# Kernel optimization log

Measured on AMD Instinct MI355X. Metric: run time of the kernel, lower is better.

## Reference

```python
import jax, jax.numpy as jnp
import numpy as np

N, NF1, NF2, NH, OUT, K = 16384, 2000, 10000, 512, 16, 19
BN_EPS = 1e-5

def _bn(x, g, b, m, v):
    # eval-mode BatchNorm1d with running stats
    return (x - m) * jax.lax.rsqrt(v + BN_EPS) * g + b


def setup_inputs() -> dict:
    key = jax.random.key(0)
    ks = jax.random.split(key, 24)
    f32 = jnp.float32
    def w(k, shape):
        return jax.random.normal(k, shape, f32) * 0.02
    inp = {
        "rna": jax.random.normal(ks[0], (N, NF1), f32),
        "atac": jax.random.normal(ks[1], (N, NF2), f32),
        "index_rna": jnp.arange(N, dtype=jnp.int32),
        "index_atac": jnp.arange(N, dtype=jnp.int32),
        "eps": jax.random.normal(ks[2], (N, OUT), f32),
        # RNA encoder
        "W_r1": w(ks[3], (NH, NF1)), "b_r1": jnp.zeros((NH,), f32),
        "g_r": jnp.ones((NH,), f32), "be_r": jnp.zeros((NH,), f32),
        "m_r": jnp.zeros((NH,), f32), "v_r": jnp.ones((NH,), f32),
        "W_rmu": w(ks[4], (OUT, NH)), "b_rmu": jnp.zeros((OUT,), f32),
        "W_rvar": w(ks[5], (OUT, NH)), "b_rvar": jnp.zeros((OUT,), f32),
        # ATAC encoder
        "W_a1": w(ks[6], (NH, NF2)), "b_a1": jnp.zeros((NH,), f32),
        "g_a": jnp.ones((NH,), f32), "be_a": jnp.zeros((NH,), f32),
        "m_a": jnp.zeros((NH,), f32), "v_a": jnp.ones((NH,), f32),
        "W_amu": w(ks[7], (OUT, NH)), "b_amu": jnp.zeros((OUT,), f32),
        "W_avar": w(ks[8], (OUT, NH)), "b_avar": jnp.zeros((OUT,), f32),
        # decoder
        "W_d1": w(ks[9], (NH, OUT)), "b_d1": jnp.zeros((NH,), f32),
        "g_d": jnp.ones((NH,), f32), "be_d": jnp.zeros((NH,), f32),
        "m_d": jnp.zeros((NH,), f32), "v_d": jnp.ones((NH,), f32),
        "W_d4": w(ks[10], (NF1 + NF2, NH)), "b_d4": jnp.zeros((NF1 + NF2,), f32),
        "cluster": jax.random.normal(ks[11], (K, OUT), f32),
    }
    return inp


def reference(rna, atac, index_rna, index_atac, eps,
              W_r1, b_r1, g_r, be_r, m_r, v_r, W_rmu, b_rmu, W_rvar, b_rvar,
              W_a1, b_a1, g_a, be_a, m_a, v_a, W_amu, b_amu, W_avar, b_avar,
              W_d1, b_d1, g_d, be_d, m_d, v_d, W_d4, b_d4, cluster):
    n = rna.shape[0]
    # encoders (dropout is identity in eval mode)
    h_rna = jax.nn.relu(_bn(rna @ W_r1.T + b_r1, g_r, be_r, m_r, v_r))
    zm_rna = h_rna @ W_rmu.T + b_rmu
    zv_rna = jnp.exp(h_rna @ W_rvar.T + b_rvar)
    h_atac = jax.nn.relu(_bn(atac @ W_a1.T + b_a1, g_a, be_a, m_a, v_a))
    zm_atac = h_atac @ W_amu.T + b_amu
    zv_atac = jnp.exp(h_atac @ W_avar.T + b_avar)
    # vectorized scatter replacing the per-sample Python loop
    mu = jnp.ones((n, 2, OUT), rna.dtype)
    var = jnp.ones((n, 2, OUT), rna.dtype)
    mask = jnp.zeros((n, 2, OUT), rna.dtype)
    mu = mu.at[index_rna, 0].set(zm_rna).at[index_atac, 1].set(zm_atac)
    var = var.at[index_rna, 0].set(zv_rna).at[index_atac, 1].set(zv_atac)
    mask = mask.at[index_rna, 0].set(1.0).at[index_atac, 1].set(1.0)
    # product of experts over the modality axis (axis=1)
    T = mask / var
    T_sum = T.sum(axis=1) + 1.0            # [n, OUT]
    z_mu = (mu * T).sum(axis=1) / T_sum
    z_var = 1.0 / T_sum
    # Normal(z_mu, scale=z_var).rsample() with externally supplied eps
    z = z_mu + z_var * eps
    # student-t style soft assignment to clusters
    d2 = jnp.sum((z[:, None, :] - cluster[None, :, :]) ** 2, axis=2)  # [n, K]
    q = 1.0 / (1.0 + d2)
    q = q / q.sum(axis=1, keepdims=True)
    # decoder
    h = jax.nn.relu(_bn(z @ W_d1.T + b_d1, g_d, be_d, m_d, v_d))
    recon_x = h @ W_d4.T + b_d4
    return (recon_x, z_mu, z_var, z, q)
```

## Files before the change

### kernel.cpp

```cpp
#include <hip/hip_runtime.h>
#include <hip/hip_bf16.h>

#define NS    16384
#define NF1c  2000
#define NF2c  10000
#define NH    512
#define KC    19
#define NREC  12000
#define NRECP 12032

typedef short bf16x8 __attribute__((ext_vector_type(8)));
typedef float f32x4  __attribute__((ext_vector_type(4)));

__device__ __forceinline__ unsigned short f2bf(float x) {
    return __builtin_bit_cast(unsigned short, __hip_bfloat16(x));
}
__device__ __forceinline__ float bf2f(unsigned short h) {
    return __builtin_bit_cast(float, (unsigned int)h << 16);
}

__device__ __forceinline__ void sync_nodrain() {
    asm volatile("s_waitcnt lgkmcnt(0)" ::: "memory");
    __builtin_amdgcn_s_barrier();
    asm volatile("" ::: "memory");
}

template<int BK> __device__ __forceinline__ int swz(int r) {
    return (BK == 32) ? ((r >> 1) & 3) : (r & 7);
}

__device__ __forceinline__ void gload16(const unsigned short* g, unsigned short* l) {
    __builtin_amdgcn_global_load_lds(
        (const __attribute__((address_space(1))) void*)g,
        (__attribute__((address_space(3))) void*)l, 16, 0, 0);
}

__global__ void k_cvt(const float* __restrict__ s, unsigned short* __restrict__ d, int n4) {
    int i = blockIdx.x * blockDim.x + threadIdx.x;
    int st = gridDim.x * blockDim.x;
    for (; i < n4; i += st) {
        float4 f = ((const float4*)s)[i];
        ushort4 o;
        o.x = f2bf(f.x); o.y = f2bf(f.y); o.z = f2bf(f.z); o.w = f2bf(f.w);
        ((ushort4*)d)[i] = o;
    }
}

__global__ void k_cvt_pad(const float* __restrict__ s, unsigned short* __restrict__ d,
                          int K, int Rv, long nchunks) {
    long i = (long)blockIdx.x * blockDim.x + threadIdx.x;
    const long stp = (long)gridDim.x * blockDim.x;
    const int Kp8 = K / 8;
    for (; i < nchunks; i += stp) {
        const long row = i / Kp8;
        const int  col = (int)(i - row * Kp8) * 8;
        __align__(16) unsigned short u[8] = {0, 0, 0, 0, 0, 0, 0, 0};
        if (row < Rv) {
            const float* p = s + row * (long)K + col;
            float4 f0 = *(const float4*)p;
            float4 f1 = *(const float4*)(p + 4);
            u[0] = f2bf(f0.x); u[1] = f2bf(f0.y); u[2] = f2bf(f0.z); u[3] = f2bf(f0.w);
            u[4] = f2bf(f1.x); u[5] = f2bf(f1.y); u[6] = f2bf(f1.z); u[7] = f2bf(f1.w);
        }
        *(uint4*)(d + row * (long)K + col) = *(uint4*)u;
    }
}

__global__ void k_prep_st(const float* __restrict__ g, const float* __restrict__ be,
                          const float* __restrict__ m, const float* __restrict__ v,
                          const float* __restrict__ b1,
                          float* __restrict__ s, float* __restrict__ t, int n) {
    int i = blockIdx.x * blockDim.x + threadIdx.x;
    if (i < n) {
        float sc = g[i] * rsqrtf(v[i] + 1e-5f);
        s[i] = sc;
        t[i] = be[i] + (b1[i] - m[i]) * sc;
    }
}

__global__ void k_zero(float* __restrict__ p, int n) {
    int i = blockIdx.x * blockDim.x + threadIdx.x;
    if (i < n) p[i] = 0.f;
}

__global__ __launch_bounds__(256)
void k_gemm(const void* __restrict__ Aptr, const unsigned short* __restrict__ B,
            int K, int Nn, int ntn,
            const float* __restrict__ sc, const float* __restrict__ sh,
            unsigned short* __restrict__ Hout)
{
    constexpr int BK = 64;
    constexpr int JC = BK / 16;
    __shared__ __align__(16) unsigned short As[2][128 * BK];
    __shared__ __align__(16) unsigned short Bs[2][128 * BK];

    const int nwg = gridDim.x;
    const int q8  = nwg >> 3;
    const int L   = (blockIdx.x & 7) * q8 + (blockIdx.x >> 3);
    const int tn  = L % ntn, tm = L / ntn;

    const int tid  = threadIdx.x;
    const int wave = tid >> 6, lane = tid & 63;
    const int wr   = wave >> 1, wc = wave & 1;
    const int lo   = lane & 15, hi = lane >> 4;
    const int srow = tid >> 1, shalf = tid & 1;
    const long arow = (long)tm * 128 + srow;
    const int  brow = tn * 128 + srow;
    const bool bok  = (brow < Nn);

    const float*          Af = (const float*)Aptr + arow * (long)K;
    const unsigned short* Bp = B + (long)brow * K;

    f32x4 acc[4][4];
#pragma unroll
    for (int i = 0; i < 4; i++)
#pragma unroll
        for (int j = 0; j < 4; j++) acc[i][j] = (f32x4){0.f, 0.f, 0.f, 0.f};

    float4 rfa[BK / 8];
    uint4  rb[JC];

    auto issue = [&](int k0, bool tail) {
        const int kb = k0 + shalf * (BK / 2);
        if (!tail) {
#pragma unroll
            for (int q = 0; q < BK / 8; q++) rfa[q] = *(const float4*)(Af + kb + q * 4);
        } else {
#pragma unroll
            for (int q = 0; q < BK / 8; q++) {
                float4 f;
                f.x = (kb + q * 4 + 0 < K) ? Af[kb + q * 4 + 0] : 0.f;
                f.y = (kb + q * 4 + 1 < K) ? Af[kb + q * 4 + 1] : 0.f;
                f.z = (kb + q * 4 + 2 < K) ? Af[kb + q * 4 + 2] : 0.f;
                f.w = (kb + q * 4 + 3 < K) ? Af[kb + q * 4 + 3] : 0.f;
                rfa[q] = f;
            }
        }
#pragma unroll
        for (int j = 0; j < JC; j++) rb[j] = (uint4){0, 0, 0, 0};
        if (bok) {
            if (!tail) {
#pragma unroll
                for (int j = 0; j < JC; j++) rb[j] = *(const uint4*)(Bp + kb + j * 8);
            } else {
#pragma unroll
                for (int j = 0; j < JC; j++) {
                    __align__(16) unsigned short t8[8];
#pragma unroll
                    for (int e = 0; e < 8; e++)
                        t8[e] = (kb + j * 8 + e < K) ? Bp[kb + j * 8 + e] : (unsigned short)0;
                    rb[j] = *(uint4*)t8;
                }
            }
        }
    };

    auto write = [&](int buf) {
        char* Ap = (char*)As[buf];
        char* Bq = (char*)Bs[buf];
        const int rbase = srow * (2 * BK);
        const int sw = swz<BK>(srow);
#pragma unroll
        for (int j = 0; j < JC; j++) {
            const int c = shalf * JC + j;
            const int pos = rbase + ((c ^ sw) << 4);
            uint4 av;
            unsigned int* w32 = (unsigned int*)&av;
            const float* fp = (const float*)&rfa[2 * j];
#pragma unroll
            for (int e = 0; e < 4; e++) {
                unsigned int l16 = f2bf(fp[2 * e]);
                unsigned int h16 = f2bf(fp[2 * e + 1]);
                w32[e] = l16 | (h16 << 16);
            }
            *(uint4*)(Ap + pos) = av;
            *(uint4*)(Bq + pos) = rb[j];
        }
    };

    auto comp = [&](int buf) {
        const char* Ap = (const char*)As[buf];
        const char* Bq = (const char*)Bs[buf];
#pragma unroll
        for (int s = 0; s < BK / 32; s++) {
            bf16x8 af[4], bfv[4];
#pragma unroll
            for (int f = 0; f < 4; f++) {
                const int ar = wr * 64 + f * 16 + lo;
                af[f]  = *(const bf16x8*)(Ap + ar * (2 * BK) + (((s * 4 + hi) ^ swz<BK>(ar)) << 4));
                const int br = wc * 64 + f * 16 + lo;
                bfv[f] = *(const bf16x8*)(Bq + br * (2 * BK) + (((s * 4 + hi) ^ swz<BK>(br)) << 4));
            }
#pragma unroll
            for (int i = 0; i < 4; i++)
#pragma unroll
                for (int j = 0; j < 4; j++)
                    acc[i][j] = __builtin_amdgcn_mfma_f32_16x16x32_bf16(af[i], bfv[j], acc[i][j], 0, 0, 0);
        }
    };

    const int ntf = K / BK;
    const bool rem = (K % BK) != 0;
    const int nt = ntf + (rem ? 1 : 0);
    issue(0, rem && nt == 1);
    for (int t = 0; t < nt; ++t) {
        write(t & 1);
        if (t + 1 < nt) issue((t + 1) * BK, rem && (t + 1 == nt - 1));
        sync_nodrain();
        comp(t & 1);
    }

#pragma unroll
    for (int i = 0; i < 4; i++) {
#pragma unroll
        for (int j = 0; j < 4; j++) {
            const int col = tn * 128 + wc * 64 + j * 16 + lo;
#pragma unroll
            for (int r = 0; r < 4; r++) {
                const long row = (long)tm * 128 + wr * 64 + i * 16 + hi * 4 + r;
                float v = fmaxf(acc[i][j][r] * sc[col] + sh[col], 0.f);
                Hout[row * NH + col] = f2bf(v);
            }
        }
    }
}

__global__ __launch_bounds__(512)
void k_rec256(const unsigned short* __restrict__ A, const unsigned short* __restrict__ B,
              const float* __restrict__ bias, float* __restrict__ Fout)
{
    __shared__ __align__(16) unsigned short As[2][256 * 32];
    __shared__ __align__(16) unsigned short Bs[2][256 * 32];

    const int q8 = gridDim.x >> 3;
    const int L  = (blockIdx.x & 7) * q8 + (blockIdx.x >> 3);
    const int tn = L % 47, tm = L / 47;

    const int tid  = threadIdx.x;
    const int w    = tid >> 6, lane = tid & 63;
    const int wm   = w >> 2, wn = w & 3;
    const int lo   = lane & 15, hi = lane >> 4;

    const int rl0 = w * 32 + (lane >> 2);
    const int sch = ((lane & 3) ^ ((lane >> 3) & 3)) * 8;
    const unsigned short* Adma = A + (size_t)(tm * 256 + rl0) * NH + sch;
    const unsigned short* Bdma = B + (size_t)(tn * 256 + rl0) * NH + sch;

    f32x4 acc[8][4];
#pragma unroll
    for (int i = 0; i < 8; i++)
#pragma unroll
        for (int j = 0; j < 4; j++) acc[i][j] = (f32x4){0.f, 0.f, 0.f, 0.f};

    auto issue = [&](int buf, int kt) {
        const int ko = kt * 32;
        gload16(Adma + ko,            &As[buf][(w * 32) * 32]);
        gload16(Adma + 16 * NH + ko,  &As[buf][(w * 32 + 16) * 32]);
        gload16(Bdma + ko,            &Bs[buf][(w * 32) * 32]);
        gload16(Bdma + 16 * NH + ko,  &Bs[buf][(w * 32 + 16) * 32]);
    };
    auto ldA = [&](int buf, int fm) -> bf16x8 {
        const int ar = wm * 128 + fm * 16 + lo;
        return *(const bf16x8*)((const char*)As[buf] + ar * 64 + ((hi ^ ((ar >> 1) & 3)) << 4));
    };
    auto ldB = [&](int buf, int fn) -> bf16x8 {
        const int br = wn * 64 + fn * 16 + lo;
        return *(const bf16x8*)((const char*)Bs[buf] + br * 64 + ((hi ^ ((br >> 1) & 3)) << 4));
    };

    const int nt = NH / 32;
    issue(0, 0);
    asm volatile("s_waitcnt vmcnt(0)" ::: "memory");
    __builtin_amdgcn_s_barrier();
    asm volatile("" ::: "memory");

    for (int kt = 0; kt < nt; ++kt) {
        const int cur = kt & 1;
        const bool more = (kt + 1 < nt);
        if (more) issue(cur ^ 1, kt + 1);
        bf16x8 bf[4], a0, a1, a2, a3;
#pragma unroll
        for (int fn = 0; fn < 4; fn++) bf[fn] = ldB(cur, fn);
        a0 = ldA(cur, 0); a1 = ldA(cur, 1); a2 = ldA(cur, 2); a3 = ldA(cur, 3);
        asm volatile("s_waitcnt lgkmcnt(0)" ::: "memory");
        __builtin_amdgcn_s_setprio(1);
#pragma unroll
        for (int fn = 0; fn < 4; fn++) {
            acc[0][fn] = __builtin_amdgcn_mfma_f32_16x16x32_bf16(a0, bf[fn], acc[0][fn], 0, 0, 0);
            acc[1][fn] = __builtin_amdgcn_mfma_f32_16x16x32_bf16(a1, bf[fn], acc[1][fn], 0, 0, 0);
            acc[2][fn] = __builtin_amdgcn_mfma_f32_16x16x32_bf16(a2, bf[fn], acc[2][fn], 0, 0, 0);
            acc[3][fn] = __builtin_amdgcn_mfma_f32_16x16x32_bf16(a3, bf[fn], acc[3][fn], 0, 0, 0);
        }
        __builtin_amdgcn_s_setprio(0);
        a0 = ldA(cur, 4); a1 = ldA(cur, 5); a2 = ldA(cur, 6); a3 = ldA(cur, 7);
        asm volatile("s_waitcnt lgkmcnt(0)" ::: "memory");
        __builtin_amdgcn_s_setprio(1);
#pragma unroll
        for (int fn = 0; fn < 4; fn++) {
            acc[4][fn] = __builtin_amdgcn_mfma_f32_16x16x32_bf16(a0, bf[fn], acc[4][fn], 0, 0, 0);
            acc[5][fn] = __builtin_amdgcn_mfma_f32_16x16x32_bf16(a1, bf[fn], acc[5][fn], 0, 0, 0);
            acc[6][fn] = __builtin_amdgcn_mfma_f32_16x16x32_bf16(a2, bf[fn], acc[6][fn], 0, 0, 0);
            acc[7][fn] = __builtin_amdgcn_mfma_f32_16x16x32_bf16(a3, bf[fn], acc[7][fn], 0, 0, 0);
        }
        __builtin_amdgcn_s_setprio(0);
        if (more) {
            asm volatile("s_waitcnt vmcnt(0)" ::: "memory");
            __builtin_amdgcn_s_barrier();
            asm volatile("" ::: "memory");
        }
    }

#pragma unroll
    for (int fm = 0; fm < 8; fm++) {
#pragma unroll
        for (int fn = 0; fn < 4; fn++) {
            const int col = tn * 256 + wn * 64 + fn * 16 + lo;
#pragma unroll
            for (int r = 0; r < 4; r++) {
                const long row = (long)tm * 256 + wm * 128 + fm * 16 + hi * 4 + r;
                if (col < NREC) Fout[row * (long)NREC + col] = acc[fm][fn][r] + bias[col];
            }
        }
    }
}

__global__ __launch_bounds__(256)
void k_proj(const unsigned short* __restrict__ h_rna,
            const unsigned short* __restrict__ h_atac,
            const float* __restrict__ W_rmu, const float* __restrict__ b_rmu,
            const float* __restrict__ W_rvar, const float* __restrict__ b_rvar,
            const float* __restrict__ W_amu, const float* __restrict__ b_amu,
            const float* __restrict__ W_avar, const float* __restrict__ b_avar,
            const int* __restrict__ idx_rna, const int* __restrict__ idx_atac,
            float* __restrict__ mu0, float* __restrict__ var0,
            float* __restrict__ mu1, float* __restrict__ var1,
            float* __restrict__ mflag)
{
    __shared__ __align__(16) unsigned short hsh[4][2][NH];
    const int wave = threadIdx.x >> 6, lane = threadIdx.x & 63;
    const long i = (long)blockIdx.x * 4 + wave;
    *(uint4*)&hsh[wave][0][lane * 8] = *(const uint4*)(h_rna  + i * NH + lane * 8);
    *(uint4*)&hsh[wave][1][lane * 8] = *(const uint4*)(h_atac + i * NH + lane * 8);
    __syncthreads();
    const int mod = lane >> 5, oo = lane & 31;
    const int isv = oo >> 4, o = oo & 15;
    const float *W, *bias;
    if (mod == 0) { W = isv ? W_rvar : W_rmu; bias = isv ? b_rvar : b_rmu; }
    else          { W = isv ? W_avar : W_amu; bias = isv ? b_avar : b_amu; }
    const unsigned short* hr = hsh[wave][mod];
    const float* wrow = W + o * NH;
    float a = 0.f;
#pragma unroll 4
    for (int k = 0; k < NH; k += 4) {
        float4 w = *(const float4*)(wrow + k);
        a += bf2f(hr[k]) * w.x + bf2f(hr[k+1]) * w.y + bf2f(hr[k+2]) * w.z + bf2f(hr[k+3]) * w.w;
    }
    a += bias[o];
    const int tgt = (mod == 0) ? idx_rna[i] : idx_atac[i];
    float* mu  = mod ? mu1  : mu0;
    float* var = mod ? var1 : var0;
    if (!isv) mu[(long)tgt * 16 + o] = a;
    else      var[(long)tgt * 16 + o] = expf(a);
    if (oo == 0) mflag[(long)mod * NS + tgt] = 1.f;
}

__global__ __launch_bounds__(256)
void k_combine(const float* __restrict__ mu0, const float* __restrict__ var0,
               const float* __restrict__ mu1, const float* __restrict__ var1,
               const float* __restrict__ mflag,
               const float* __restrict__ eps, const float* __restrict__ cluster,
               const float* __restrict__ W_d1,
               const float* __restrict__ s_d, const float* __restrict__ t_d,
               float* __restrict__ o_zmu, float* __restrict__ o_zvar,
               float* __restrict__ o_z, float* __restrict__ o_q,
               unsigned short* __restrict__ h_d)
{
    __shared__ float zsh[4][16];
    const int wave = threadIdx.x >> 6, lane = threadIdx.x & 63;
    const long i = (long)blockIdx.x * 4 + wave;
    if (lane < 16) {
        const int d = lane;
        const float f0 = mflag[i], f1 = mflag[NS + i];
        float ts = 1.f, num = 0.f;
        if (f0 != 0.f) { float iv = 1.f / var0[i*16+d]; ts += iv; num += mu0[i*16+d] * iv; }
        if (f1 != 0.f) { float iv = 1.f / var1[i*16+d]; ts += iv; num += mu1[i*16+d] * iv; }
        const float zm = num / ts, zv = 1.f / ts;
        const float z = zm + zv * eps[i*16+d];
        o_zmu[i*16+d] = zm; o_zvar[i*16+d] = zv; o_z[i*16+d] = z;
        zsh[wave][d] = z;
    }
    __syncthreads();
    float zreg[16];
#pragma unroll
    for (int d = 0; d < 16; d++) zreg[d] = zsh[wave][d];
    float qk = 0.f;
    if (lane < KC) {
        float d2 = 0.f;
#pragma unroll
        for (int d = 0; d < 16; d++) { float df = zreg[d] - cluster[lane*16+d]; d2 += df*df; }
        qk = 1.f / (1.f + d2);
    }
    float ssum = qk;
#pragma unroll
    for (int off = 16; off > 0; off >>= 1) ssum += __shfl_xor(ssum, off, 32);
    if (lane < KC) o_q[i * KC + lane] = qk / ssum;
#pragma unroll
    for (int j = 0; j < 8; j++) {
        const int c = lane + 64 * j;
        float a = 0.f;
#pragma unroll
        for (int d = 0; d < 16; d += 4) {
            float4 w = *(const float4*)(W_d1 + c * 16 + d);
            a += zreg[d] * w.x + zreg[d+1] * w.y + zreg[d+2] * w.z + zreg[d+3] * w.w;
        }
        a = fmaxf(a * s_d[c] + t_d[c], 0.f);
        h_d[i * NH + c] = f2bf(a);
    }
}

extern "C" void kernel_launch(void* const* d_in, const int* in_sizes, int n_in,
                              void* d_out, int out_size, void* d_ws, size_t ws_size,
                              hipStream_t stream)
{
    const float* rna    = (const float*)d_in[0];
    const float* atac   = (const float*)d_in[1];
    const int*   i_rna  = (const int*)d_in[2];
    const int*   i_atac = (const int*)d_in[3];
    const float* eps    = (const float*)d_in[4];
    const float* W_r1   = (const float*)d_in[5];
    const float* b_r1   = (const float*)d_in[6];
    const float* g_r    = (const float*)d_in[7];
    const float* be_r   = (const float*)d_in[8];
    const float* m_r    = (const float*)d_in[9];
    const float* v_r    = (const float*)d_in[10];
    const float* W_rmu  = (const float*)d_in[11];
    const float* b_rmu  = (const float*)d_in[12];
    const float* W_rvar = (const float*)d_in[13];
    const float* b_rvar = (const float*)d_in[14];
    const float* W_a1   = (const float*)d_in[15];
    const float* b_a1   = (const float*)d_in[16];
    const float* g_a    = (const float*)d_in[17];
    const float* be_a   = (const float*)d_in[18];
    const float* m_a    = (const float*)d_in[19];
    const float* v_a    = (const float*)d_in[20];
    const float* W_amu  = (const float*)d_in[21];
    const float* b_amu  = (const float*)d_in[22];
    const float* W_avar = (const float*)d_in[23];
    const float* b_avar = (const float*)d_in[24];
    const float* W_d1   = (const float*)d_in[25];
    const float* b_d1   = (const float*)d_in[26];
    const float* g_d    = (const float*)d_in[27];
    const float* be_d   = (const float*)d_in[28];
    const float* m_d    = (const float*)d_in[29];
    const float* v_d    = (const float*)d_in[30];
    const float* W_d4   = (const float*)d_in[31];
    const float* b_d4   = (const float*)d_in[32];
    const float* clus   = (const float*)d_in[33];
    (void)in_sizes; (void)n_in; (void)out_size;

    char* w = (char*)d_ws;
    size_t off = 0;
    auto carve = [&](size_t bytes) { void* p = w + off; off += (bytes + 255) & ~(size_t)255; return p; };
    unsigned short* wr1b  = (unsigned short*)carve((size_t)NH * NF1c * 2);
    unsigned short* wa1b  = (unsigned short*)carve((size_t)NH * NF2c * 2);
    unsigned short* wd4b  = (unsigned short*)carve((size_t)NRECP * NH * 2);
    unsigned short* hrna  = (unsigned short*)carve((size_t)NS * NH * 2);
    unsigned short* hatac = (unsigned short*)carve((size_t)NS * NH * 2);
    unsigned short* hd    = (unsigned short*)carve((size_t)NS * NH * 2);
    float* mu0   = (float*)carve((size_t)NS * 16 * 4);
    float* var0  = (float*)carve((size_t)NS * 16 * 4);
    float* mu1   = (float*)carve((size_t)NS * 16 * 4);
    float* var1  = (float*)carve((size_t)NS * 16 * 4);
    float* mflag = (float*)carve((size_t)2 * NS * 4);
    float* st    = (float*)carve((size_t)6 * NH * 4);
    if (off > ws_size) return;

    float* s_r = st;          float* t_r = st + NH;
    float* s_a = st + 2*NH;   float* t_a = st + 3*NH;
    float* s_d = st + 4*NH;   float* t_d = st + 5*NH;

    float* out    = (float*)d_out;
    float* o_rec  = out;
    float* o_zmu  = out + (size_t)NS * NREC;
    float* o_zvar = o_zmu + (size_t)NS * 16;
    float* o_z    = o_zvar + (size_t)NS * 16;
    float* o_q    = o_z + (size_t)NS * 16;

    k_cvt<<<1024, 256, 0, stream>>>(W_r1, wr1b, NH * NF1c / 4);
    k_cvt<<<2048, 256, 0, stream>>>(W_a1, wa1b, NH * NF2c / 4);
    k_cvt_pad<<<2048, 256, 0, stream>>>(W_d4, wd4b, NH, NREC, (long)NRECP * (NH / 8));
    k_prep_st<<<2, 256, 0, stream>>>(g_r, be_r, m_r, v_r, b_r1, s_r, t_r, NH);
    k_prep_st<<<2, 256, 0, stream>>>(g_a, be_a, m_a, v_a, b_a1, s_a, t_a, NH);
    k_prep_st<<<2, 256, 0, stream>>>(g_d, be_d, m_d, v_d, b_d1, s_d, t_d, NH);
    k_zero<<<(2 * NS + 255) / 256, 256, 0, stream>>>(mflag, 2 * NS);

    dim3 blk(256);
    k_gemm<<<512, blk, 0, stream>>>(rna,  wr1b, NF1c, NH, 4, s_r, t_r, hrna);
    k_gemm<<<512, blk, 0, stream>>>(atac, wa1b, NF2c, NH, 4, s_a, t_a, hatac);
    k_proj<<<NS / 4, blk, 0, stream>>>(hrna, hatac, W_rmu, b_rmu, W_rvar, b_rvar,
                                       W_amu, b_amu, W_avar, b_avar, i_rna, i_atac,
                                       mu0, var0, mu1, var1, mflag);
    k_combine<<<NS / 4, blk, 0, stream>>>(mu0, var0, mu1, var1, mflag, eps, clus,
                                          W_d1, s_d, t_d, o_zmu, o_zvar, o_z, o_q, hd);
    k_rec256<<<3008, dim3(512), 0, stream>>>(hd, wd4b, b_d4, o_rec);
}
```

Before: 1.201 ms.

## Fuse both encoder GEMMs into one launch and load B fragments directly to registers

The two encoder GEMMs (RNA K=2000, ATAC K=10000) are merged into a single 1024-block launch, with blocks interleaved between the two problems so the short RNA tiles fill in around the long ATAC tiles. The B (weight) operand no longer goes through shared memory. Each lane loads its MFMA fragment straight from global memory into registers, double-buffered across the two k-substeps. This cuts LDS traffic and footprint and removes the tail imbalance of two separate launches, at the cost of uncoalesced per-lane global loads for B and more register pressure.

```diff
diff --git a/kernel.cpp b/kernel.cpp
--- a/kernel.cpp
+++ b/kernel.cpp
@@ -84,32 +84,40 @@
 }
 
 __global__ __launch_bounds__(256)
-void k_gemm(const void* __restrict__ Aptr, const unsigned short* __restrict__ B,
-            int K, int Nn, int ntn,
-            const float* __restrict__ sc, const float* __restrict__ sh,
-            unsigned short* __restrict__ Hout)
+void k_encf(const float* __restrict__ A_a, const float* __restrict__ A_r,
+            const unsigned short* __restrict__ B_a, const unsigned short* __restrict__ B_r,
+            const float* __restrict__ s_a, const float* __restrict__ t_a,
+            const float* __restrict__ s_r, const float* __restrict__ t_r,
+            unsigned short* __restrict__ H_a, unsigned short* __restrict__ H_r)
 {
     constexpr int BK = 64;
-    constexpr int JC = BK / 16;
     __shared__ __align__(16) unsigned short As[2][128 * BK];
-    __shared__ __align__(16) unsigned short Bs[2][128 * BK];
-
-    const int nwg = gridDim.x;
-    const int q8  = nwg >> 3;
-    const int L   = (blockIdx.x & 7) * q8 + (blockIdx.x >> 3);
-    const int tn  = L % ntn, tm = L / ntn;
+
+    const int q8 = gridDim.x >> 3;
+    const int L  = (blockIdx.x & 7) * q8 + (blockIdx.x >> 3);
+    const int which = L & 1;
+    const int inner = L >> 1;
+    const int tn = inner & 3, tm = inner >> 2;
+
+    const float*          Ag = which ? A_r : A_a;
+    const unsigned short* Bg = which ? B_r : B_a;
+    const int K = which ? NF1c : NF2c;
+    const float* sc = which ? s_r : s_a;
+    const float* sh = which ? t_r : t_a;
+    unsigned short* Hout = which ? H_r : H_a;
 
     const int tid  = threadIdx.x;
     const int wave = tid >> 6, lane = tid & 63;
     const int wr   = wave >> 1, wc = wave & 1;
     const int lo   = lane & 15, hi = lane >> 4;
     const int srow = tid >> 1, shalf = tid & 1;
-    const long arow = (long)tm * 128 + srow;
-    const int  brow = tn * 128 + srow;
-    const bool bok  = (brow < Nn);
-
-    const float*          Af = (const float*)Aptr + arow * (long)K;
-    const unsigned short* Bp = B + (long)brow * K;
+
+    const float* Af = Ag + (size_t)(tm * 128 + srow) * K;
+
+    const unsigned short* Brow0 = Bg + (size_t)(tn * 128 + wc * 64 +  0 + lo) * K + hi * 8;
+    const unsigned short* Brow1 = Bg + (size_t)(tn * 128 + wc * 64 + 16 + lo) * K + hi * 8;
+    const unsigned short* Brow2 = Bg + (size_t)(tn * 128 + wc * 64 + 32 + lo) * K + hi * 8;
+    const unsigned short* Brow3 = Bg + (size_t)(tn * 128 + wc * 64 + 48 + lo) * K + hi * 8;
 
     f32x4 acc[4][4];
 #pragma unroll
@@ -118,9 +126,9 @@
         for (int j = 0; j < 4; j++) acc[i][j] = (f32x4){0.f, 0.f, 0.f, 0.f};
 
     float4 rfa[BK / 8];
-    uint4  rb[JC];
-
-    auto issue = [&](int k0, bool tail) {
+    bf16x8 b0[4], b1[4];
+
+    auto issueA = [&](int k0, bool tail) {
         const int kb = k0 + shalf * (BK / 2);
         if (!tail) {
 #pragma unroll
@@ -136,34 +144,15 @@
                 rfa[q] = f;
             }
         }
-#pragma unroll
-        for (int j = 0; j < JC; j++) rb[j] = (uint4){0, 0, 0, 0};
-        if (bok) {
-            if (!tail) {
-#pragma unroll
-                for (int j = 0; j < JC; j++) rb[j] = *(const uint4*)(Bp + kb + j * 8);
-            } else {
-#pragma unroll
-                for (int j = 0; j < JC; j++) {
-                    __align__(16) unsigned short t8[8];
-#pragma unroll
-                    for (int e = 0; e < 8; e++)
-                        t8[e] = (kb + j * 8 + e < K) ? Bp[kb + j * 8 + e] : (unsigned short)0;
-                    rb[j] = *(uint4*)t8;
-                }
-            }
-        }
-    };
-
-    auto write = [&](int buf) {
+    };
+
+    auto writeA = [&](int buf) {
         char* Ap = (char*)As[buf];
-        char* Bq = (char*)Bs[buf];
         const int rbase = srow * (2 * BK);
         const int sw = swz<BK>(srow);
 #pragma unroll
-        for (int j = 0; j < JC; j++) {
-            const int c = shalf * JC + j;
-            const int pos = rbase + ((c ^ sw) << 4);
+        for (int j = 0; j < BK / 16; j++) {
+            const int c = shalf * (BK / 16) + j;
             uint4 av;
             unsigned int* w32 = (unsigned int*)&av;
             const float* fp = (const float*)&rfa[2 * j];
@@ -173,41 +162,62 @@
                 unsigned int h16 = f2bf(fp[2 * e + 1]);
                 w32[e] = l16 | (h16 << 16);
             }
-            *(uint4*)(Ap + pos) = av;
-            *(uint4*)(Bq + pos) = rb[j];
-        }
-    };
-
-    auto comp = [&](int buf) {
+            *(uint4*)(Ap + rbase + ((c ^ sw) << 4)) = av;
+        }
+    };
+
+    auto loadB = [&](bf16x8* dst, int kb, bool tail) {
+        if (!tail) {
+            dst[0] = *(const bf16x8*)(Brow0 + kb);
+            dst[1] = *(const bf16x8*)(Brow1 + kb);
+            dst[2] = *(const bf16x8*)(Brow2 + kb);
+            dst[3] = *(const bf16x8*)(Brow3 + kb);
+        } else {
+            const int c0 = kb + hi * 8;
+            bf16x8 v0 = {}, v1 = {}, v2 = {}, v3 = {};
+#pragma unroll
+            for (int e = 0; e < 8; e++) {
+                if (c0 + e < K) {
+                    ((short*)&v0)[e] = ((const short*)(Brow0 + kb))[e];
+                    ((short*)&v1)[e] = ((const short*)(Brow1 + kb))[e];
+                    ((short*)&v2)[e] = ((const short*)(Brow2 + kb))[e];
+                    ((short*)&v3)[e] = ((const short*)(Brow3 + kb))[e];
+                }
+            }
+            dst[0] = v0; dst[1] = v1; dst[2] = v2; dst[3] = v3;
+        }
+    };
+
+    auto compS = [&](int buf, int s, const bf16x8* bfv) {
         const char* Ap = (const char*)As[buf];
-        const char* Bq = (const char*)Bs[buf];
-#pragma unroll
-        for (int s = 0; s < BK / 32; s++) {
-            bf16x8 af[4], bfv[4];
-#pragma unroll
-            for (int f = 0; f < 4; f++) {
-                const int ar = wr * 64 + f * 16 + lo;
-                af[f]  = *(const bf16x8*)(Ap + ar * (2 * BK) + (((s * 4 + hi) ^ swz<BK>(ar)) << 4));
-                const int br = wc * 64 + f * 16 + lo;
-                bfv[f] = *(const bf16x8*)(Bq + br * (2 * BK) + (((s * 4 + hi) ^ swz<BK>(br)) << 4));
-            }
-#pragma unroll
-            for (int i = 0; i < 4; i++)
-#pragma unroll
-                for (int j = 0; j < 4; j++)
-                    acc[i][j] = __builtin_amdgcn_mfma_f32_16x16x32_bf16(af[i], bfv[j], acc[i][j], 0, 0, 0);
-        }
+        bf16x8 af[4];
+#pragma unroll
+        for (int f = 0; f < 4; f++) {
+            const int ar = wr * 64 + f * 16 + lo;
+            af[f] = *(const bf16x8*)(Ap + ar * (2 * BK) + (((s * 4 + hi) ^ swz<BK>(ar)) << 4));
+        }
+#pragma unroll
+        for (int i = 0; i < 4; i++)
+#pragma unroll
+            for (int j = 0; j < 4; j++)
+                acc[i][j] = __builtin_amdgcn_mfma_f32_16x16x32_bf16(af[i], bfv[j], acc[i][j], 0, 0, 0);
     };
 
     const int ntf = K / BK;
     const bool rem = (K % BK) != 0;
     const int nt = ntf + (rem ? 1 : 0);
-    issue(0, rem && nt == 1);
+
+    issueA(0, rem && nt == 1);
+    loadB(b0, 0, false);
     for (int t = 0; t < nt; ++t) {
-        write(t & 1);
-        if (t + 1 < nt) issue((t + 1) * BK, rem && (t + 1 == nt - 1));
+        const int k0 = t * BK;
+        writeA(t & 1);
+        if (t + 1 < nt) issueA((t + 1) * BK, rem && (t + 1 == nt - 1));
+        loadB(b1, k0 + 32, k0 + 64 > K);
         sync_nodrain();
-        comp(t & 1);
+        compS(t & 1, 0, b0);
+        if (t + 1 < nt) loadB(b0, (t + 1) * BK, (t + 1) * BK + 32 > K);
+        compS(t & 1, 1, b1);
     }
 
 #pragma unroll
@@ -495,8 +505,8 @@
     k_zero<<<(2 * NS + 255) / 256, 256, 0, stream>>>(mflag, 2 * NS);
 
     dim3 blk(256);
-    k_gemm<<<512, blk, 0, stream>>>(rna,  wr1b, NF1c, NH, 4, s_r, t_r, hrna);
-    k_gemm<<<512, blk, 0, stream>>>(atac, wa1b, NF2c, NH, 4, s_a, t_a, hatac);
+    k_encf<<<1024, blk, 0, stream>>>(atac, rna, wa1b, wr1b,
+                                     s_a, t_a, s_r, t_r, hatac, hrna);
     k_proj<<<NS / 4, blk, 0, stream>>>(hrna, hatac, W_rmu, b_rmu, W_rvar, b_rvar,
                                        W_amu, b_amu, W_avar, b_avar, i_rna, i_atac,
                                        mu0, var0, mu1, var1, mflag);
```

Result: slower. 1.567 ms (+30.4%).
